# Kernel optimization log

Hardware: AMD Instinct MI355X
Metric: run time of the kernel (lower is better)

The kernel has to match this reference:

```python
import jax, jax.numpy as jnp
import numpy as np

B, C, D_IN, T = 8, 4, 256, 1024
D_MODEL = 256


def setup_inputs() -> dict:
    key = jax.random.key(0)
    k_x, k_m, k_wq, k_bq, k_wo, k_bo = jax.random.split(key, 6)
    x = jax.random.normal(k_x, (B, C, D_IN, T), dtype=jnp.float32)
    mask = jax.random.randint(k_m, (B, C, T, T), 0, 2) == 1  # bool, True = masked
    s_in = 1.0 / np.sqrt(D_IN)
    s_md = 1.0 / np.sqrt(D_MODEL)
    w_qkv = jax.random.uniform(k_wq, (3 * D_MODEL, D_IN), jnp.float32, -s_in, s_in)
    b_qkv = jax.random.uniform(k_bq, (3 * D_MODEL,), jnp.float32, -s_in, s_in)
    w_out = jax.random.uniform(k_wo, (D_MODEL, D_MODEL), jnp.float32, -s_md, s_md)
    b_out = jax.random.uniform(k_bo, (D_MODEL,), jnp.float32, -s_md, s_md)
    return {"x": x, "mask": mask, "w_qkv": w_qkv, "b_qkv": b_qkv,
            "w_out": w_out, "b_out": b_out}


def reference(x, mask, w_qkv, b_qkv, w_out, b_out):
    # x: (B, C, d_in, t) -> (B, C, t, d_in)
    xt = jnp.swapaxes(x, -1, -2)
    qkv = jnp.einsum('bctd,ed->bcte', xt, w_qkv) + b_qkv  # (B,C,t,3*d_model)
    q, k, v = jnp.split(qkv, 3, axis=-1)
    scale = 1.0 / jnp.sqrt(jnp.asarray(q.shape[-1], dtype=q.dtype))
    scores = jnp.einsum('bcqd,bckd->bcqk', q, k) * scale  # (B,C,t,t)
    scores = jnp.where(mask, -jnp.inf, scores)
    attn = jax.nn.softmax(scores, axis=-1)
    out = jnp.einsum('bcqk,bckd->bcqd', attn, v)          # (B,C,t,d_model)
    return jnp.einsum('bcqd,ed->bcqe', out, w_out) + b_out
```

## Files before the change

### kernel.cpp

```cpp
#include <hip/hip_runtime.h>
#include <hip/hip_bf16.h>

#define TT 1024
#define DM 256
#define BCN 32

typedef __attribute__((ext_vector_type(8))) short short8;
typedef __attribute__((ext_vector_type(4))) short short4v;
typedef __attribute__((ext_vector_type(4))) float f32x4;

__device__ __forceinline__ void wg_barrier_lds() {
  asm volatile("s_waitcnt lgkmcnt(0)\n\ts_barrier" ::: "memory");
}

__device__ __forceinline__ short bf16b(float f) {
  __hip_bfloat16 h = __float2bfloat16(f);
  return *(short*)&h;
}

__device__ __forceinline__ void dma16(void* l, const void* g) {
  __builtin_amdgcn_global_load_lds(
      (const __attribute__((address_space(1))) void*)g,
      (__attribute__((address_space(3))) void*)l, 16, 0, 0);
}
__device__ __forceinline__ void dma4(void* l, const void* g) {
  __builtin_amdgcn_global_load_lds(
      (const __attribute__((address_space(1))) void*)g,
      (__attribute__((address_space(3))) void*)l, 4, 0, 0);
}

__global__ __launch_bounds__(256) void prep_kernel(
    const float* __restrict__ w_qkv, __hip_bfloat16* __restrict__ Wb)
{
  const int idx = blockIdx.x * 256 + threadIdx.x;
  const int r = idx >> 5, ch = idx & 31;
  const float4* wv4 = (const float4*)w_qkv + (size_t)r * 64 + ch * 2;
  const float4 f0 = wv4[0], f1 = wv4[1];
  short8 pk;
  pk[0] = bf16b(f0.x); pk[1] = bf16b(f0.y);
  pk[2] = bf16b(f0.z); pk[3] = bf16b(f0.w);
  pk[4] = bf16b(f1.x); pk[5] = bf16b(f1.y);
  pk[6] = bf16b(f1.z); pk[7] = bf16b(f1.w);
  *(short8*)&Wb[(size_t)r * 256 + ((ch ^ (r & 7)) << 3)] = pk;
}

__global__ __launch_bounds__(256, 8) void mask_kernel(
    const int* __restrict__ mask, unsigned* __restrict__ mbits)
{
  const int tid = threadIdx.x;
  __shared__ unsigned Wlds[64][33];
  const int m = blockIdx.x;
  const int bc = m >> 4, q0 = (m & 15) * 64;
  const int w = tid >> 6, l = tid & 63;
  const int4* base =
      (const int4*)(mask + (size_t)(bc * 1024 + q0 + w * 16) * 1024) + l;
  int4 v[4], n[4];
#pragma unroll
  for (int s = 0; s < 4; ++s) v[s] = base[s * 64];
#pragma unroll 1
  for (int rr = 0; rr < 16; ++rr) {
    if (rr < 15) {
      const int4* nb = base + (rr + 1) * 256;
#pragma unroll
      for (int s = 0; s < 4; ++s) n[s] = nb[s * 64];
    }
    const int ql = w * 16 + rr;
#pragma unroll
    for (int s = 0; s < 4; ++s) {
      const unsigned long long bx = __ballot(v[s].x != 0);
      const unsigned long long by = __ballot(v[s].y != 0);
      const unsigned long long bz = __ballot(v[s].z != 0);
      const unsigned long long bw = __ballot(v[s].w != 0);
      if (l < 8) {
        const unsigned word =
            (unsigned)((bx >> (8 * l)) & 0xFF) |
            ((unsigned)((by >> (8 * l)) & 0xFF) << 8) |
            ((unsigned)((bz >> (8 * l)) & 0xFF) << 16) |
            ((unsigned)((bw >> (8 * l)) & 0xFF) << 24);
        Wlds[ql][s * 8 + l] = word;
      }
    }
#pragma unroll
    for (int s = 0; s < 4; ++s) v[s] = n[s];
  }
  __syncthreads();
  unsigned* mb = mbits + (size_t)bc * 32 * 1024 + q0;
#pragma unroll
  for (int i = 0; i < 8; ++i) {
    const int idx = tid + i * 256, j = idx >> 6, ql = idx & 63;
    mb[(size_t)j * 1024 + ql] = Wlds[ql][j];
  }
}

__global__ __launch_bounds__(256, 2) void qkv_kernel(
    const float* __restrict__ x, const __hip_bfloat16* __restrict__ Wb,
    const float* __restrict__ b_qkv,
    __hip_bfloat16* __restrict__ Qb, __hip_bfloat16* __restrict__ Kb,
    __hip_bfloat16* __restrict__ Vtb)
{
  const int tid = threadIdx.x;

  __shared__ __attribute__((aligned(16))) __hip_bfloat16 Xs[64][264];
  __shared__ __attribute__((aligned(16))) __hip_bfloat16 Wd[2][32 * 256];
  __shared__ __attribute__((aligned(16))) float bls[768];

  const int tt = blockIdx.x & 15, bc = blockIdx.x >> 4;
  const int t0 = tt * 64;
  const int w = tid >> 6, l = tid & 63, quad = l >> 4, lm = l & 15;
  const int lm7 = lm & 7;

  const char* Wg = (const char*)Wb;
  auto wissue = [&](int it, int buf) {
    const char* g = Wg + (size_t)it * 16384 + w * 4096 + l * 16;
    char* d = (char*)&Wd[buf][0] + w * 4096;
#pragma unroll
    for (int i = 0; i < 4; ++i) dma16(d + i * 1024, g + i * 1024);
  };

  wissue(0, 0);
  wissue(1, 1);

  if (tid < 192) {
    const float4 bv = *(const float4*)(b_qkv + tid * 4);
    *(float4*)&bls[tid * 4] = bv;
  }

  {
    const float* xbc = x + (size_t)bc * DM * TT;
    const int t4 = (tid & 15) * 4;
    for (int s = 0; s < 4; ++s) {
      const int d4 = (tid >> 4) * 4 + s * 64;
      f32x4 f[4];
#pragma unroll
      for (int r = 0; r < 4; ++r)
        f[r] = *(const f32x4*)(xbc + (size_t)(d4 + r) * TT + t0 + t4);
#pragma unroll
      for (int r = 0; r < 4; ++r) {
        short4v pk;
#pragma unroll
        for (int c = 0; c < 4; ++c) pk[c] = bf16b(f[c][r]);
        *(short4v*)&Xs[t4 + r][d4] = pk;
      }
    }
  }

#pragma unroll 1
  for (int it = 0; it < 24; ++it) {
    const int buf = it & 1;
    if (it == 0)
      asm volatile("s_waitcnt vmcnt(4)" ::: "memory");
    else if (it < 23)
      asm volatile("s_waitcnt vmcnt(6)" ::: "memory");
    else
      asm volatile("s_waitcnt vmcnt(2)" ::: "memory");
    wg_barrier_lds();

    const int e0 = it * 32;
    const bool vmode = (it >= 16);
    const __hip_bfloat16* WT = &Wd[buf][0];
    f32x4 acc[2] = {};
#pragma unroll
    for (int ks = 0; ks < 8; ++ks) {
      const int k = ks * 32 + quad * 8;
      const short8 xa = *(const short8*)&Xs[w * 16 + lm][k];
      const int c = ((ks * 4 + quad) ^ lm7) << 3;
#pragma unroll
      for (int nt = 0; nt < 2; ++nt) {
        const short8 wb2 = *(const short8*)&WT[(nt * 16 + lm) * 256 + c];
        acc[nt] = vmode
            ? __builtin_amdgcn_mfma_f32_16x16x32_bf16(xa, wb2, acc[nt], 0, 0, 0)
            : __builtin_amdgcn_mfma_f32_16x16x32_bf16(wb2, xa, acc[nt], 0, 0, 0);
      }
    }

    if (it < 8) {
      const int t = t0 + w * 16 + lm;
#pragma unroll
      for (int nt = 0; nt < 2; ++nt) {
        const int ebase = e0 + nt * 16 + quad * 4;
        const f32x4 bb = *(const f32x4*)&bls[ebase];
        short4v pk;
#pragma unroll
        for (int r = 0; r < 4; ++r) pk[r] = bf16b(acc[nt][r] + bb[r]);
        *(short4v*)&Qb[((size_t)bc * TT + t) * DM + ebase] = pk;
      }
    } else if (!vmode) {
      const int t = t0 + w * 16 + lm;
#pragma unroll
      for (int nt = 0; nt < 2; ++nt) {
        const int eg = e0 + nt * 16 + quad * 4;
        const int eK = eg - 256;
        const f32x4 bb = *(const f32x4*)&bls[eg];
        short4v pk;
#pragma unroll
        for (int r = 0; r < 4; ++r) pk[r] = bf16b(acc[nt][r] + bb[r]);
        const int ch = eK >> 3;
        const int off = (((ch ^ (t & 7)) << 3) | (eK & 7));
        *(short4v*)&Kb[((size_t)bc * TT + t) * DM + off] = pk;
      }
    } else {
      const int tb = w * 16 + quad * 4;
      const int kb = tt * 2 + (tb >> 5), tloc = tb & 31;
#pragma unroll
      for (int nt = 0; nt < 2; ++nt) {
        const int e = (e0 - 512) + nt * 16 + lm;
        const float bq = bls[512 + e];
        short4v pk;
#pragma unroll
        for (int r = 0; r < 4; ++r) pk[r] = bf16b(acc[nt][r] + bq);
        *(short4v*)&Vtb[(((size_t)bc * 32 + kb) * 256 + e) * 32 + tloc] = pk;
      }
    }

    wg_barrier_lds();
    if (it < 22) wissue(it + 2, buf);
  }
}

__global__ __launch_bounds__(256, 2) void attn_kernel(
    const __hip_bfloat16* __restrict__ Qb, const __hip_bfloat16* __restrict__ Kb,
    const __hip_bfloat16* __restrict__ Vtb, const unsigned* __restrict__ Mbits,
    __hip_bfloat16* __restrict__ Ob)
{
  const int fid = blockIdx.x;
  const int xcd = fid & 7, slot = fid >> 3;
  const int bc = xcd * 4 + (slot >> 4);
  const int qt = slot & 15;
  const int q0 = qt * 64;

  __shared__ __attribute__((aligned(16))) __hip_bfloat16 Ks[2][32 * 256];
  __shared__ __attribute__((aligned(16))) __hip_bfloat16 Vs[2][256 * 32];
  __shared__ __attribute__((aligned(16))) __hip_bfloat16 Ps[64][40];
  __shared__ unsigned Msb[2][64];

  const int tid = threadIdx.x, w = tid >> 6, l = tid & 63;
  const int quad = l >> 4, lm = l & 15, lm7 = lm & 7;

  const __hip_bfloat16* Qg =
      Qb + ((size_t)bc * TT + q0 + w * 16 + lm) * DM + quad * 8;
  short8 qf[8];
#pragma unroll
  for (int ks = 0; ks < 8; ++ks) qf[ks] = *(const short8*)(Qg + ks * 32);

  const char* KgT = (const char*)(Kb + (size_t)bc * TT * DM);
  const char* VgT = (const char*)(Vtb + (size_t)bc * TT * DM);
  const unsigned* MgT = Mbits + ((size_t)bc * 32) * 1024 + q0;

  short8 ones;
#pragma unroll
  for (int i = 0; i < 8; ++i) ones[i] = (short)0x3F80;

  f32x4 Oa[16] = {};
  f32x4 Ol = {};

  auto issue = [&](int j, int buf) {
    const char* kg = KgT + (size_t)j * 16384 + w * 4096 + l * 16;
    const char* vg = VgT + (size_t)j * 16384 + w * 4096 + l * 16;
    char* kl = (char*)&Ks[buf][0] + w * 4096;
    char* vl = (char*)&Vs[buf][0] + w * 4096;
#pragma unroll
    for (int i = 0; i < 4; ++i) dma16(kl + i * 1024, kg + i * 1024);
#pragma unroll
    for (int i = 0; i < 4; ++i) dma16(vl + i * 1024, vg + i * 1024);
    dma4(&Msb[buf][0], MgT + (size_t)j * 1024 + l);
  };

  auto compute = [&](int buf) {
    const __hip_bfloat16* KT = &Ks[buf][0];
    const __hip_bfloat16* VT = &Vs[buf][0];
    f32x4 Sa0 = {}, Sa1 = {};
#pragma unroll
    for (int ks = 0; ks < 8; ++ks) {
      const int c = ((ks * 4 + quad) ^ lm7) << 3;
      const short8 a0 = *(const short8*)&KT[lm * 256 + c];
      const short8 a1 = *(const short8*)&KT[(lm + 16) * 256 + c];
      Sa0 = __builtin_amdgcn_mfma_f32_16x16x32_bf16(a0, qf[ks], Sa0, 0, 0, 0);
      Sa1 = __builtin_amdgcn_mfma_f32_16x16x32_bf16(a1, qf[ks], Sa1, 0, 0, 0);
    }
    const unsigned mw = Msb[buf][w * 16 + lm];
#pragma unroll
    for (int nt = 0; nt < 2; ++nt) {
      const f32x4 Sa = nt ? Sa1 : Sa0;
      short4v pk;
#pragma unroll
      for (int r = 0; r < 4; ++r) {
        const float p = ((mw >> (nt * 4 + quad + 8 * r)) & 1u)
                            ? 0.f
                            : __expf(fmaf(Sa[r], 0.0625f, -8.0f));
        pk[r] = bf16b(p);
      }
      *(short4v*)&Ps[w * 16 + lm][nt * 16 + quad * 4] = pk;
    }
    const short8 pf = *(const short8*)&Ps[w * 16 + lm][quad * 8];
#pragma unroll
    for (int ct = 0; ct < 16; ++ct) {
      const short8 a = *(const short8*)&VT[(ct * 16 + lm) * 32 + quad * 8];
      Oa[ct] = __builtin_amdgcn_mfma_f32_16x16x32_bf16(a, pf, Oa[ct], 0, 0, 0);
    }
    Ol = __builtin_amdgcn_mfma_f32_16x16x32_bf16(ones, pf, Ol, 0, 0, 0);
  };

  issue(0, 0);
  issue(1, 1);
#pragma unroll 1
  for (int j = 0; j < 32; ++j) {
    const int buf = j & 1;
    if (j < 31)
      asm volatile("s_waitcnt vmcnt(9)" ::: "memory");
    else
      asm volatile("s_waitcnt vmcnt(0)" ::: "memory");
    asm volatile("s_barrier" ::: "memory");
    compute(buf);
    wg_barrier_lds();
    if (j < 30) issue(j + 2, buf);
  }

  const float inv = 1.0f / Ol[0];
  __hip_bfloat16* Og = Ob + ((size_t)bc * TT + q0 + w * 16 + lm) * DM;
#pragma unroll
  for (int ct = 0; ct < 16; ++ct) {
    short4v pk;
#pragma unroll
    for (int r = 0; r < 4; ++r) pk[r] = bf16b(Oa[ct][r] * inv);
    *(short4v*)&Og[ct * 16 + quad * 4] = pk;
  }
}

__global__ __launch_bounds__(256, 2) void proj_kernel(
    const __hip_bfloat16* __restrict__ Ob, const float* __restrict__ w_out,
    const float* __restrict__ b_out, float* __restrict__ out)
{
  const int ft = blockIdx.x, tt = blockIdx.y, bc = blockIdx.z;
  const int f0 = ft * 64, t0 = tt * 64;

  __shared__ __attribute__((aligned(16))) __hip_bfloat16 As[64][264];
  __shared__ __attribute__((aligned(16))) __hip_bfloat16 Bs[64][264];

  const int tid = threadIdx.x;
  const uint4* Og4 = (const uint4*)(Ob + ((size_t)bc * TT + t0) * DM);
#pragma unroll
  for (int i = 0; i < 8; ++i) {
    const int chunk = tid + i * 256, row = chunk >> 5, c8 = chunk & 31;
    *(uint4*)&As[row][c8 * 8] = Og4[chunk];
  }
  {
    const float4* wv = (const float4*)(w_out + (size_t)f0 * DM);
#pragma unroll
    for (int i = 0; i < 16; ++i) {
      const int idx = tid + i * 256, row = idx >> 6, c4 = idx & 63;
      const float4 f = wv[idx];
      short4v pk;
      pk[0] = bf16b(f.x); pk[1] = bf16b(f.y);
      pk[2] = bf16b(f.z); pk[3] = bf16b(f.w);
      *(short4v*)&Bs[row][c4 * 4] = pk;
    }
  }
  __syncthreads();

  const int w = tid >> 6, l = tid & 63, quad = l >> 4, lm = l & 15;
  f32x4 acc[4] = {};
#pragma unroll
  for (int ks = 0; ks < 8; ++ks) {
    const int k = ks * 32 + quad * 8;
    const short8 ob = *(const short8*)&As[w * 16 + lm][k];
#pragma unroll
    for (int nt = 0; nt < 4; ++nt) {
      const short8 wa = *(const short8*)&Bs[nt * 16 + lm][k];
      acc[nt] = __builtin_amdgcn_mfma_f32_16x16x32_bf16(wa, ob, acc[nt], 0, 0, 0);
    }
  }
  const int t = t0 + w * 16 + lm;
#pragma unroll
  for (int nt = 0; nt < 4; ++nt) {
    const int fb = f0 + nt * 16 + quad * 4;
    float4 o;
    o.x = acc[nt][0] + b_out[fb + 0];
    o.y = acc[nt][1] + b_out[fb + 1];
    o.z = acc[nt][2] + b_out[fb + 2];
    o.w = acc[nt][3] + b_out[fb + 3];
    *(float4*)&out[((size_t)bc * TT + t) * DM + fb] = o;
  }
}

extern "C" void kernel_launch(void* const* d_in, const int* in_sizes, int n_in,
                              void* d_out, int out_size, void* d_ws, size_t ws_size,
                              hipStream_t stream) {
  const float* x = (const float*)d_in[0];
  const int* mask = (const int*)d_in[1];
  const float* w_qkv = (const float*)d_in[2];
  const float* b_qkv = (const float*)d_in[3];
  const float* w_out = (const float*)d_in[4];
  const float* b_out = (const float*)d_in[5];
  float* out = (float*)d_out;

  const size_t N = (size_t)BCN * TT * DM;
  __hip_bfloat16* Qb  = (__hip_bfloat16*)d_ws;
  __hip_bfloat16* Kb  = Qb + N;
  __hip_bfloat16* Vtb = Kb + N;
  unsigned* Mbits     = (unsigned*)(Vtb + N);
  __hip_bfloat16* Wbp = (__hip_bfloat16*)(Mbits + (size_t)BCN * 32 * 1024);

  prep_kernel<<<dim3(96), dim3(256), 0, stream>>>(w_qkv, Wbp);
  mask_kernel<<<dim3(512), dim3(256), 0, stream>>>(mask, Mbits);
  qkv_kernel<<<dim3(512), dim3(256), 0, stream>>>(x, Wbp, b_qkv, Qb, Kb, Vtb);
  attn_kernel<<<dim3(512), dim3(256), 0, stream>>>(Qb, Kb, Vtb, Mbits, Qb);
  proj_kernel<<<dim3(4, 16, BCN), dim3(256), 0, stream>>>(Qb, w_out, b_out, out);
}
```

Before: 342.6 us.

## Fuse output projection into attention kernel epilogue with pipelined weight tiles

Removes the separate projection kernel. Each attention block now stages its normalized bf16 output tile in LDS, keeps it in registers, and multiplies it against a pre-swizzled bf16 w_out that the prep kernel produces. Those weight slices are double-buffered through async global-to-LDS loads. This avoids writing and re-reading the attention output through global memory, avoids one launch, and avoids converting w_out per block. In exchange the attention kernel gets a longer tail and reuses LDS, which may affect occupancy.

```diff
diff --git a/kernel.cpp b/kernel.cpp
--- a/kernel.cpp
+++ b/kernel.cpp
@@ -30,18 +30,23 @@
 }
 
 __global__ __launch_bounds__(256) void prep_kernel(
-    const float* __restrict__ w_qkv, __hip_bfloat16* __restrict__ Wb)
+    const float* __restrict__ w_qkv, const float* __restrict__ w_out,
+    __hip_bfloat16* __restrict__ Wb, __hip_bfloat16* __restrict__ Wo)
 {
-  const int idx = blockIdx.x * 256 + threadIdx.x;
+  int idx = blockIdx.x * 256 + threadIdx.x;
+  const float* src;
+  __hip_bfloat16* dst;
+  if (idx < 24576) { src = w_qkv; dst = Wb; }
+  else { idx -= 24576; src = w_out; dst = Wo; }
   const int r = idx >> 5, ch = idx & 31;
-  const float4* wv4 = (const float4*)w_qkv + (size_t)r * 64 + ch * 2;
+  const float4* wv4 = (const float4*)src + (size_t)r * 64 + ch * 2;
   const float4 f0 = wv4[0], f1 = wv4[1];
   short8 pk;
   pk[0] = bf16b(f0.x); pk[1] = bf16b(f0.y);
   pk[2] = bf16b(f0.z); pk[3] = bf16b(f0.w);
   pk[4] = bf16b(f1.x); pk[5] = bf16b(f1.y);
   pk[6] = bf16b(f1.z); pk[7] = bf16b(f1.w);
-  *(short8*)&Wb[(size_t)r * 256 + ((ch ^ (r & 7)) << 3)] = pk;
+  *(short8*)&dst[(size_t)r * 256 + ((ch ^ (r & 7)) << 3)] = pk;
 }
 
 __global__ __launch_bounds__(256, 8) void mask_kernel(
@@ -220,7 +225,8 @@
 __global__ __launch_bounds__(256, 2) void attn_kernel(
     const __hip_bfloat16* __restrict__ Qb, const __hip_bfloat16* __restrict__ Kb,
     const __hip_bfloat16* __restrict__ Vtb, const unsigned* __restrict__ Mbits,
-    __hip_bfloat16* __restrict__ Ob)
+    const __hip_bfloat16* __restrict__ Wob, const float* __restrict__ b_out,
+    float* __restrict__ out)
 {
   const int fid = blockIdx.x;
   const int xcd = fid & 7, slot = fid >> 3;
@@ -228,16 +234,26 @@
   const int qt = slot & 15;
   const int q0 = qt * 64;
 
-  __shared__ __attribute__((aligned(16))) __hip_bfloat16 Ks[2][32 * 256];
-  __shared__ __attribute__((aligned(16))) __hip_bfloat16 Vs[2][256 * 32];
-  __shared__ __attribute__((aligned(16))) __hip_bfloat16 Ps[64][40];
-  __shared__ unsigned Msb[2][64];
+  __shared__ __attribute__((aligned(16))) char smem[72192];
+  __hip_bfloat16* Ks = (__hip_bfloat16*)smem;
+  __hip_bfloat16* Vs = (__hip_bfloat16*)(smem + 32768);
+  __hip_bfloat16 (*Ps)[40] = (__hip_bfloat16(*)[40])(smem + 65536);
+  unsigned* Msb = (unsigned*)(smem + 70656);
+  float* bout = (float*)(smem + 71168);
+  __hip_bfloat16 (*Os)[264] = (__hip_bfloat16(*)[264])smem;
+  __hip_bfloat16* Wo = (__hip_bfloat16*)(smem + 33792);
 
   const int tid = threadIdx.x, w = tid >> 6, l = tid & 63;
   const int quad = l >> 4, lm = l & 15, lm7 = lm & 7;
+  const int trow = w * 16 + lm;
+
+  if (tid < 64) {
+    const f32x4 bv = *(const f32x4*)(b_out + tid * 4);
+    *(f32x4*)&bout[tid * 4] = bv;
+  }
 
   const __hip_bfloat16* Qg =
-      Qb + ((size_t)bc * TT + q0 + w * 16 + lm) * DM + quad * 8;
+      Qb + ((size_t)bc * TT + q0 + trow) * DM + quad * 8;
   short8 qf[8];
 #pragma unroll
   for (int ks = 0; ks < 8; ++ks) qf[ks] = *(const short8*)(Qg + ks * 32);
@@ -256,18 +272,18 @@
   auto issue = [&](int j, int buf) {
     const char* kg = KgT + (size_t)j * 16384 + w * 4096 + l * 16;
     const char* vg = VgT + (size_t)j * 16384 + w * 4096 + l * 16;
-    char* kl = (char*)&Ks[buf][0] + w * 4096;
-    char* vl = (char*)&Vs[buf][0] + w * 4096;
+    char* kl = (char*)Ks + buf * 16384 + w * 4096;
+    char* vl = (char*)Vs + buf * 16384 + w * 4096;
 #pragma unroll
     for (int i = 0; i < 4; ++i) dma16(kl + i * 1024, kg + i * 1024);
 #pragma unroll
     for (int i = 0; i < 4; ++i) dma16(vl + i * 1024, vg + i * 1024);
-    dma4(&Msb[buf][0], MgT + (size_t)j * 1024 + l);
+    dma4((char*)Msb + buf * 256, MgT + (size_t)j * 1024 + l);
   };
 
   auto compute = [&](int buf) {
-    const __hip_bfloat16* KT = &Ks[buf][0];
-    const __hip_bfloat16* VT = &Vs[buf][0];
+    const __hip_bfloat16* KT = Ks + buf * 8192;
+    const __hip_bfloat16* VT = Vs + buf * 8192;
     f32x4 Sa0 = {}, Sa1 = {};
 #pragma unroll
     for (int ks = 0; ks < 8; ++ks) {
@@ -277,7 +293,7 @@
       Sa0 = __builtin_amdgcn_mfma_f32_16x16x32_bf16(a0, qf[ks], Sa0, 0, 0, 0);
       Sa1 = __builtin_amdgcn_mfma_f32_16x16x32_bf16(a1, qf[ks], Sa1, 0, 0, 0);
     }
-    const unsigned mw = Msb[buf][w * 16 + lm];
+    const unsigned mw = Msb[buf * 64 + trow];
 #pragma unroll
     for (int nt = 0; nt < 2; ++nt) {
       const f32x4 Sa = nt ? Sa1 : Sa0;
@@ -289,9 +305,9 @@
                             : __expf(fmaf(Sa[r], 0.0625f, -8.0f));
         pk[r] = bf16b(p);
       }
-      *(short4v*)&Ps[w * 16 + lm][nt * 16 + quad * 4] = pk;
-    }
-    const short8 pf = *(const short8*)&Ps[w * 16 + lm][quad * 8];
+      *(short4v*)&Ps[trow][nt * 16 + quad * 4] = pk;
+    }
+    const short8 pf = *(const short8*)&Ps[trow][quad * 8];
 #pragma unroll
     for (int ct = 0; ct < 16; ++ct) {
       const short8 a = *(const short8*)&VT[(ct * 16 + lm) * 32 + quad * 8];
@@ -316,69 +332,66 @@
   }
 
   const float inv = 1.0f / Ol[0];
-  __hip_bfloat16* Og = Ob + ((size_t)bc * TT + q0 + w * 16 + lm) * DM;
 #pragma unroll
   for (int ct = 0; ct < 16; ++ct) {
     short4v pk;
 #pragma unroll
     for (int r = 0; r < 4; ++r) pk[r] = bf16b(Oa[ct][r] * inv);
-    *(short4v*)&Og[ct * 16 + quad * 4] = pk;
-  }
-}
-
-__global__ __launch_bounds__(256, 2) void proj_kernel(
-    const __hip_bfloat16* __restrict__ Ob, const float* __restrict__ w_out,
-    const float* __restrict__ b_out, float* __restrict__ out)
-{
-  const int ft = blockIdx.x, tt = blockIdx.y, bc = blockIdx.z;
-  const int f0 = ft * 64, t0 = tt * 64;
-
-  __shared__ __attribute__((aligned(16))) __hip_bfloat16 As[64][264];
-  __shared__ __attribute__((aligned(16))) __hip_bfloat16 Bs[64][264];
-
-  const int tid = threadIdx.x;
-  const uint4* Og4 = (const uint4*)(Ob + ((size_t)bc * TT + t0) * DM);
-#pragma unroll
-  for (int i = 0; i < 8; ++i) {
-    const int chunk = tid + i * 256, row = chunk >> 5, c8 = chunk & 31;
-    *(uint4*)&As[row][c8 * 8] = Og4[chunk];
-  }
-  {
-    const float4* wv = (const float4*)(w_out + (size_t)f0 * DM);
-#pragma unroll
-    for (int i = 0; i < 16; ++i) {
-      const int idx = tid + i * 256, row = idx >> 6, c4 = idx & 63;
-      const float4 f = wv[idx];
-      short4v pk;
-      pk[0] = bf16b(f.x); pk[1] = bf16b(f.y);
-      pk[2] = bf16b(f.z); pk[3] = bf16b(f.w);
-      *(short4v*)&Bs[row][c4 * 4] = pk;
-    }
-  }
-  __syncthreads();
-
-  const int w = tid >> 6, l = tid & 63, quad = l >> 4, lm = l & 15;
-  f32x4 acc[4] = {};
-#pragma unroll
-  for (int ks = 0; ks < 8; ++ks) {
-    const int k = ks * 32 + quad * 8;
-    const short8 ob = *(const short8*)&As[w * 16 + lm][k];
-#pragma unroll
-    for (int nt = 0; nt < 4; ++nt) {
-      const short8 wa = *(const short8*)&Bs[nt * 16 + lm][k];
-      acc[nt] = __builtin_amdgcn_mfma_f32_16x16x32_bf16(wa, ob, acc[nt], 0, 0, 0);
-    }
-  }
-  const int t = t0 + w * 16 + lm;
-#pragma unroll
-  for (int nt = 0; nt < 4; ++nt) {
-    const int fb = f0 + nt * 16 + quad * 4;
-    float4 o;
-    o.x = acc[nt][0] + b_out[fb + 0];
-    o.y = acc[nt][1] + b_out[fb + 1];
-    o.z = acc[nt][2] + b_out[fb + 2];
-    o.w = acc[nt][3] + b_out[fb + 3];
-    *(float4*)&out[((size_t)bc * TT + t) * DM + fb] = o;
+    *(short4v*)&Os[trow][ct * 16 + quad * 4] = pk;
+  }
+  wg_barrier_lds();
+
+  short8 osr[8];
+#pragma unroll
+  for (int ks = 0; ks < 8; ++ks)
+    osr[ks] = *(const short8*)&Os[trow][ks * 32 + quad * 8];
+
+  const char* WoG = (const char*)Wob;
+  auto pissue = [&](int it, int buf) {
+    const char* g = WoG + (size_t)it * 16384 + w * 4096 + l * 16;
+    char* d = (char*)Wo + buf * 16384 + w * 4096;
+#pragma unroll
+    for (int i = 0; i < 4; ++i) dma16(d + i * 1024, g + i * 1024);
+  };
+  pissue(0, 0);
+  pissue(1, 1);
+
+  float* outp = out + ((size_t)bc * TT + q0 + trow) * DM;
+#pragma unroll 1
+  for (int it = 0; it < 8; ++it) {
+    const int buf = it & 1;
+    if (it == 0)
+      asm volatile("s_waitcnt vmcnt(4)" ::: "memory");
+    else if (it < 7)
+      asm volatile("s_waitcnt vmcnt(6)" ::: "memory");
+    else
+      asm volatile("s_waitcnt vmcnt(2)" ::: "memory");
+    wg_barrier_lds();
+
+    f32x4 acc[2] = {};
+#pragma unroll
+    for (int ks = 0; ks < 8; ++ks) {
+      const int c = ((ks * 4 + quad) ^ lm7) << 3;
+#pragma unroll
+      for (int nt = 0; nt < 2; ++nt) {
+        const short8 wa = *(const short8*)&Wo[buf * 8192 + (nt * 16 + lm) * 256 + c];
+        acc[nt] = __builtin_amdgcn_mfma_f32_16x16x32_bf16(wa, osr[ks], acc[nt], 0, 0, 0);
+      }
+    }
+#pragma unroll
+    for (int nt = 0; nt < 2; ++nt) {
+      const int fb = it * 32 + nt * 16 + quad * 4;
+      const f32x4 bb = *(const f32x4*)&bout[fb];
+      float4 o;
+      o.x = acc[nt][0] + bb[0];
+      o.y = acc[nt][1] + bb[1];
+      o.z = acc[nt][2] + bb[2];
+      o.w = acc[nt][3] + bb[3];
+      *(float4*)&outp[fb] = o;
+    }
+
+    wg_barrier_lds();
+    if (it < 6) pissue(it + 2, buf);
   }
 }
 
@@ -399,10 +412,11 @@
   __hip_bfloat16* Vtb = Kb + N;
   unsigned* Mbits     = (unsigned*)(Vtb + N);
   __hip_bfloat16* Wbp = (__hip_bfloat16*)(Mbits + (size_t)BCN * 32 * 1024);
-
-  prep_kernel<<<dim3(96), dim3(256), 0, stream>>>(w_qkv, Wbp);
+  __hip_bfloat16* Wob = Wbp + 768 * 256;
+
+  prep_kernel<<<dim3(128), dim3(256), 0, stream>>>(w_qkv, w_out, Wbp, Wob);
   mask_kernel<<<dim3(512), dim3(256), 0, stream>>>(mask, Mbits);
   qkv_kernel<<<dim3(512), dim3(256), 0, stream>>>(x, Wbp, b_qkv, Qb, Kb, Vtb);
-  attn_kernel<<<dim3(512), dim3(256), 0, stream>>>(Qb, Kb, Vtb, Mbits, Qb);
-  proj_kernel<<<dim3(4, 16, BCN), dim3(256), 0, stream>>>(Qb, w_out, b_out, out);
-}
+  attn_kernel<<<dim3(512), dim3(256), 0, stream>>>(Qb, Kb, Vtb, Mbits,
+                                                   Wob, b_out, out);
+}
```

New measurement: 324.7 us. 1.06x faster.
